# Kernel optimization log

Hardware: AMD Instinct MI355X
Metric: run time of the kernel (lower is better)

The kernel has to match this reference:

```python
import jax, jax.numpy as jnp
import numpy as np
import math

B, S, HID, H, WBAND = 2, 4096, 768, 12, 128
D = HID // H  # 64


def _band_qk(q, k, w):
    """q,k: [B,S,H,D] -> banded scores [B,S,H,2w+1] (offset d -> key pos i+d-w)."""
    b, s, h, d = q.shape
    nc = s // w
    kp = jnp.pad(k, ((0, 0), (w, w), (0, 0), (0, 0)))  # zero padding_value
    idx = (jnp.arange(nc) * w)[:, None] + jnp.arange(3 * w)[None, :]  # [nc,3w]
    kw = kp[:, idx]                                   # [B,nc,3w,H,D]
    qc = q.reshape(b, nc, w, h, d)
    scores = jnp.einsum('bcxhd,bcyhd->bchxy', qc, kw)  # [B,nc,H,w,3w]
    # extract diagonals: P[x,dd] = scores[x, x+dd] via flatten/skew trick
    flat = scores.reshape(b, nc, h, w * 3 * w)
    flat = jnp.pad(flat, ((0, 0), (0, 0), (0, 0), (0, w)))
    diag = flat.reshape(b, nc, h, w, 3 * w + 1)[..., : 2 * w + 1]
    return diag.transpose(0, 1, 3, 2, 4).reshape(b, s, h, 2 * w + 1)


def _band_pv(p, v, w):
    """p: [B,S,H,2w+1], v: [B,S,H,D] -> context [B,S,H,D]."""
    b, s, h, k = p.shape
    d = v.shape[-1]
    nc = s // w
    vp = jnp.pad(v, ((0, 0), (w, w), (0, 0), (0, 0)))
    idx = (jnp.arange(nc) * w)[:, None] + jnp.arange(3 * w)[None, :]
    vw = vp[:, idx]                                   # [B,nc,3w,H,D]
    pc = p.reshape(b, nc, w, h, k).transpose(0, 1, 3, 2, 4)  # [B,nc,H,w,2w+1]
    pc = jnp.pad(pc, ((0, 0), (0, 0), (0, 0), (0, 0), (0, w)))  # [..,w,3w+1]
    band = pc.reshape(b, nc, h, w * (3 * w + 1))[..., : w * 3 * w]
    band = band.reshape(b, nc, h, w, 3 * w)           # M[x, x+dd] = p[x,dd]
    ctx = jnp.einsum('bchxy,bcyhd->bcxhd', band, vw)  # [B,nc,w,H,D]
    return ctx.reshape(b, s, h, d)


def setup_inputs() -> dict:
    key = jax.random.key(0)
    ks = jax.random.split(key, 8)
    init = lambda k, shp: (jax.random.normal(k, shp, jnp.float32) * 0.02)
    return {
        'x': jax.random.normal(ks[0], (B, S, HID), jnp.float32),
        'Wq': init(ks[1], (HID, HID)), 'bq': jnp.zeros((HID,), jnp.float32),
        'Wk': init(ks[2], (HID, HID)), 'bk': jnp.zeros((HID,), jnp.float32),
        'Wv': init(ks[3], (HID, HID)), 'bv': jnp.zeros((HID,), jnp.float32),
        'Wd': init(ks[4], (H, D, HID)), 'bd': jnp.zeros((HID,), jnp.float32),
        'gamma': jnp.ones((HID,), jnp.float32),
        'beta': jnp.zeros((HID,), jnp.float32),
    }


def reference(x, Wq, bq, Wk, bk, Wv, bv, Wd, bd, gamma, beta):
    w = WBAND
    b, s, _ = x.shape
    q = (x @ Wq + bq).reshape(b, s, H, D) / math.sqrt(D)
    k = (x @ Wk + bk).reshape(b, s, H, D)
    v = (x @ Wv + bv).reshape(b, s, H, D)
    scores = _band_qk(q, k, w)                        # [B,S,H,2w+1]
    # mask_invalid_locations: key pos i + d - w must lie in [0, S)
    pos = jnp.arange(s)[:, None] + jnp.arange(2 * w + 1)[None, :] - w
    valid = (pos >= 0) & (pos < s)                    # [S,2w+1]
    scores = jnp.where(valid[None, :, None, :], scores, -1e9)
    probs = jax.nn.softmax(scores, axis=-1)           # float32 softmax
    ctx = _band_pv(probs, v, w)                       # [B,S,H,D]
    proj = jnp.einsum('bfnd,ndh->bfh', ctx, Wd) + bd  # output projection
    y = x + proj                                      # residual (dropout=0)
    mu = jnp.mean(y, axis=-1, keepdims=True)
    var = jnp.mean(jnp.square(y - mu), axis=-1, keepdims=True)
    out = (y - mu) / jnp.sqrt(var + 1e-12) * gamma + beta
    return out
```

## Files before the change

### kernel.cpp

```cpp
#include <hip/hip_runtime.h>
#include <math.h>

typedef unsigned short u16;
typedef __bf16 bf16x8 __attribute__((ext_vector_type(8)));
typedef float f32x4 __attribute__((ext_vector_type(4)));

constexpr int Bc   = 2;
constexpr int Sc   = 4096;
constexpr int HIDc = 768;
constexpr int Hc   = 12;
constexpr int Dc   = 64;
constexpr int Wc   = 128;
constexpr int Mc   = Bc * Sc;

constexpr int QT2  = 64;
constexpr int WIN  = QT2 + 2 * Wc;
constexpr int NCT  = WIN / 16;

static __device__ __forceinline__ void load_lds16(const void* g, void* l) {
    __builtin_amdgcn_global_load_lds(
        (const __attribute__((address_space(1))) void*)g,
        (__attribute__((address_space(3))) void*)l, 16, 0, 0);
}
static __device__ __forceinline__ u16 to_bf16(float f) {
    return __builtin_bit_cast(u16, (__bf16)f);
}

__global__ __launch_bounds__(256) void prep_x(const float* __restrict__ x,
                                              u16* __restrict__ xb,
                                              u16* __restrict__ zpad)
{
    int i = blockIdx.x * 256 + threadIdx.x;
    float4 v = ((const float4*)x)[i];
    ushort4 o;
    o.x = to_bf16(v.x); o.y = to_bf16(v.y);
    o.z = to_bf16(v.z); o.w = to_bf16(v.w);
    ((ushort4*)xb)[i] = o;
    if (blockIdx.x == 0 && threadIdx.x < 128)
        ((int4*)zpad)[threadIdx.x] = make_int4(0, 0, 0, 0);
}

__global__ __launch_bounds__(256) void prep_w(
    const float* __restrict__ Wq, const float* __restrict__ Wk,
    const float* __restrict__ Wv, const float* __restrict__ Wd,
    u16* __restrict__ wqt, u16* __restrict__ wkt,
    u16* __restrict__ wvt, u16* __restrict__ wdt)
{
    const int z = blockIdx.z;
    const float* W = z == 0 ? Wq : z == 1 ? Wk : z == 2 ? Wv : Wd;
    u16* T         = z == 0 ? wqt : z == 1 ? wkt : z == 2 ? wvt : wdt;

    __shared__ float t[32][33];
    const int bx = blockIdx.x * 32, by = blockIdx.y * 32;
    const int tx = threadIdx.x & 31, ty = threadIdx.x >> 5;
#pragma unroll
    for (int i = 0; i < 32; i += 8)
        t[ty + i][tx] = W[(size_t)(by + ty + i) * HIDc + bx + tx];
    __syncthreads();
#pragma unroll
    for (int i = 0; i < 32; i += 8)
        T[(size_t)(bx + ty + i) * HIDc + by + tx] = to_bf16(t[tx][ty + i]);
}

__device__ __forceinline__ void gemm128_bt(
    const u16* __restrict__ A, const u16* __restrict__ Bt,
    int m0, int n0, u16* As, u16* Bs, f32x4 (&acc)[4][4])
{
    const int tid  = threadIdx.x;
    const int lane = tid & 63, wid = tid >> 6;
    const int c16  = lane & 15, g = lane >> 4;
    const int wm   = (wid >> 1) * 64, wn = (wid & 1) * 64;
    const int soff = wid * 4096 + lane * 16;

    for (int k0 = 0; k0 < HIDc; k0 += 64) {
        __syncthreads();
#pragma unroll
        for (int i = 0; i < 4; ++i) {
            int off  = soff + i * 1024;
            int row  = off >> 7;
            int slot = (off >> 4) & 7;
            int seg  = slot ^ (row & 7);
            load_lds16(A  + (size_t)(m0 + row) * HIDc + k0 + seg * 8, (char*)As + off);
            load_lds16(Bt + (size_t)(n0 + row) * HIDc + k0 + seg * 8, (char*)Bs + off);
        }
        __syncthreads();
#pragma unroll
        for (int kk = 0; kk < 2; ++kk) {
            bf16x8 af[4], bfr[4];
#pragma unroll
            for (int t = 0; t < 4; ++t) {
                int ar = wm + t * 16 + c16;
                int as = (kk * 4 + g) ^ (ar & 7);
                af[t]  = *(const bf16x8*)(As + ar * 64 + as * 8);
                int br = wn + t * 16 + c16;
                int bs = (kk * 4 + g) ^ (br & 7);
                bfr[t] = *(const bf16x8*)(Bs + br * 64 + bs * 8);
            }
#pragma unroll
            for (int mt = 0; mt < 4; ++mt)
#pragma unroll
                for (int nt = 0; nt < 4; ++nt)
                    acc[mt][nt] = __builtin_amdgcn_mfma_f32_16x16x32_bf16(
                        af[mt], bfr[nt], acc[mt][nt], 0, 0, 0);
        }
    }
}

__global__ __launch_bounds__(256) void gemm_qkv_mfma(
    const u16* __restrict__ xb,
    const u16* __restrict__ wqt, const u16* __restrict__ wkt,
    const u16* __restrict__ wvt,
    const float* __restrict__ bq, const float* __restrict__ bk,
    const float* __restrict__ bv,
    u16* __restrict__ qg, u16* __restrict__ kg, u16* __restrict__ vtg)
{
    __shared__ u16 As[128 * 64], Bs[128 * 64];
    const int z = blockIdx.z;
    const u16* Bt     = z == 0 ? wqt : z == 1 ? wkt : wvt;
    const float* bias = z == 0 ? bq : z == 1 ? bk : bv;
    const float scale = z == 0 ? 0.125f : 1.0f;
    u16* outqk        = z == 0 ? qg : kg;

    const int m0 = blockIdx.x * 128, n0 = blockIdx.y * 128;
    f32x4 acc[4][4];
#pragma unroll
    for (int i = 0; i < 4; ++i)
#pragma unroll
        for (int j = 0; j < 4; ++j) acc[i][j] = (f32x4){0.f, 0.f, 0.f, 0.f};

    gemm128_bt(xb, Bt, m0, n0, As, Bs, acc);

    const int tid = threadIdx.x, lane = tid & 63, wid = tid >> 6;
    const int c16 = lane & 15, g = lane >> 4;
    const int wm = (wid >> 1) * 64, wn = (wid & 1) * 64;

#pragma unroll
    for (int nt = 0; nt < 4; ++nt) {
        int n = n0 + wn + nt * 16 + c16;
        int h = n >> 6, d = n & 63;
        float bn = bias[n];
#pragma unroll
        for (int mt = 0; mt < 4; ++mt) {
            int m = m0 + wm + mt * 16 + g * 4;
            int b = m >> 12, s = m & (Sc - 1);
            if (z == 2) {
                size_t base = ((size_t)(b * Hc + h)) * Sc * Dc + (size_t)d * Sc + s;
                ushort4 pk;
                pk.x = to_bf16(acc[mt][nt][0] + bn);
                pk.y = to_bf16(acc[mt][nt][1] + bn);
                pk.z = to_bf16(acc[mt][nt][2] + bn);
                pk.w = to_bf16(acc[mt][nt][3] + bn);
                *(ushort4*)&vtg[base] = pk;
            } else {
                size_t base = ((size_t)(b * Hc + h)) * Sc * Dc + (size_t)s * Dc + d;
#pragma unroll
                for (int r = 0; r < 4; ++r)
                    outqk[base + (size_t)r * Dc] =
                        to_bf16((acc[mt][nt][r] + bn) * scale);
            }
        }
    }
}

__global__ __launch_bounds__(256) void gemm_proj_mfma(
    const u16* __restrict__ ctxb, const u16* __restrict__ wdt,
    const float* __restrict__ bd, const float* __restrict__ x,
    float* __restrict__ y)
{
    __shared__ u16 As[128 * 64], Bs[128 * 64];
    const int m0 = blockIdx.x * 128, n0 = blockIdx.y * 128;
    f32x4 acc[4][4];
#pragma unroll
    for (int i = 0; i < 4; ++i)
#pragma unroll
        for (int j = 0; j < 4; ++j) acc[i][j] = (f32x4){0.f, 0.f, 0.f, 0.f};

    gemm128_bt(ctxb, wdt, m0, n0, As, Bs, acc);

    const int tid = threadIdx.x, lane = tid & 63, wid = tid >> 6;
    const int c16 = lane & 15, g = lane >> 4;
    const int wm = (wid >> 1) * 64, wn = (wid & 1) * 64;

#pragma unroll
    for (int nt = 0; nt < 4; ++nt) {
        int n = n0 + wn + nt * 16 + c16;
        float bn = bd[n];
#pragma unroll
        for (int mt = 0; mt < 4; ++mt) {
#pragma unroll
            for (int r = 0; r < 4; ++r) {
                int m = m0 + wm + mt * 16 + g * 4 + r;
                size_t idx = (size_t)m * HIDc + n;
                y[idx] = acc[mt][nt][r] + bn + x[idx];
            }
        }
    }
}

__global__ __launch_bounds__(256) void band_attn_mfma(
    const u16* __restrict__ qg, const u16* __restrict__ kg,
    const u16* __restrict__ vtg, const u16* __restrict__ zpad,
    u16* __restrict__ ctxb)
{
    extern __shared__ u16 sm[];
    u16* kwin = sm;
    u16* vt   = sm + 20480;
    u16* pm   = sm;

    const int qc = blockIdx.x, h = blockIdx.y, b = blockIdx.z;
    const int s0 = qc * QT2;
    const int tid = threadIdx.x;
    const int lane = tid & 63, wid = tid >> 6;
    const int c16 = lane & 15, g = lane >> 4;
    const size_t hb = ((size_t)(b * Hc + h)) * Sc * Dc;

#pragma unroll
    for (int i = 0; i < 10; ++i) {
        int c   = i * 4 + wid;
        int row = c * 8 + (lane >> 3);
        int seg = (lane & 7) ^ (lane >> 3);
        int pos = s0 - Wc + row;
        const u16* src = (pos >= 0 && pos < Sc)
                       ? &kg[hb + (size_t)pos * Dc + seg * 8] : zpad;
        load_lds16(src, (char*)kwin + c * 1024 + (lane & 63) * 16);
    }
#pragma unroll
    for (int i = 0; i < 10; ++i) {
        int c   = i * 4 + wid;
        int idx = c * 64 + lane;
        int d   = idx / 40;
        int p   = idx - d * 40;
        int seg = (p & 0x38) | ((p ^ d) & 7);
        int pos0 = s0 - Wc + seg * 8;
        const u16* src = (pos0 >= 0 && pos0 < Sc)
                       ? &vtg[hb + (size_t)d * Sc + pos0] : zpad;
        load_lds16(src, (char*)vt + idx * 16);
    }

    const u16* qp = &qg[hb + (size_t)(s0 + wid * 16 + c16) * Dc + g * 8];
    bf16x8 qa0 = *(const bf16x8*)qp;
    bf16x8 qa1 = *(const bf16x8*)(qp + 32);

    __syncthreads();

    f32x4 acc[NCT];
#pragma unroll
    for (int ct = 0; ct < NCT; ++ct) acc[ct] = (f32x4){0.f, 0.f, 0.f, 0.f};
    __builtin_amdgcn_s_setprio(1);
#pragma unroll
    for (int ct = 0; ct < NCT; ++ct) {
        int row = ct * 16 + c16;
        const u16* kb = kwin + row * 64;
        bf16x8 kb0 = *(const bf16x8*)(kb + (g       ^ (row & 7)) * 8);
        bf16x8 kb1 = *(const bf16x8*)(kb + ((g + 4) ^ (row & 7)) * 8);
        acc[ct] = __builtin_amdgcn_mfma_f32_16x16x32_bf16(qa0, kb0, acc[ct], 0, 0, 0);
        acc[ct] = __builtin_amdgcn_mfma_f32_16x16x32_bf16(qa1, kb1, acc[ct], 0, 0, 0);
    }
    __builtin_amdgcn_s_setprio(0);

    float mrow[4] = {-3e38f, -3e38f, -3e38f, -3e38f};
#pragma unroll
    for (int ct = 0; ct < NCT; ++ct) {
#pragma unroll
        for (int r = 0; r < 4; ++r) {
            int rl  = wid * 16 + g * 4 + r;
            int j   = ct * 16 + c16;
            int pos = s0 - Wc + j;
            bool valid = (j >= rl) && (j <= rl + 2 * Wc) && (pos >= 0) && (pos < Sc);
            float v = valid ? acc[ct][r] : -3e38f;
            acc[ct][r] = v;
            mrow[r] = fmaxf(mrow[r], v);
        }
    }
#pragma unroll
    for (int r = 0; r < 4; ++r)
#pragma unroll
        for (int off = 1; off < 16; off <<= 1)
            mrow[r] = fmaxf(mrow[r], __shfl_xor(mrow[r], off));

    float srow[4] = {0.f, 0.f, 0.f, 0.f};
#pragma unroll
    for (int ct = 0; ct < NCT; ++ct)
#pragma unroll
        for (int r = 0; r < 4; ++r) {
            float e = __expf(acc[ct][r] - mrow[r]);
            acc[ct][r] = e;
            srow[r] += e;
        }
#pragma unroll
    for (int r = 0; r < 4; ++r)
#pragma unroll
        for (int off = 1; off < 16; off <<= 1)
            srow[r] += __shfl_xor(srow[r], off);

    __syncthreads();

#pragma unroll
    for (int ct = 0; ct < NCT; ++ct)
#pragma unroll
        for (int r = 0; r < 4; ++r) {
            int q   = wid * 16 + g * 4 + r;
            int col = ct * 16 + c16;
            int sl  = col >> 3;
            int ph  = (sl & 0x38) | ((sl ^ q ^ (q >> 3)) & 7);
            pm[q * 320 + ph * 8 + (col & 7)] = to_bf16(acc[ct][r]);
        }

    f32x4 o[4];
#pragma unroll
    for (int dt = 0; dt < 4; ++dt) o[dt] = (f32x4){0.f, 0.f, 0.f, 0.f};
    const int qrow = wid * 16 + c16;
    __builtin_amdgcn_s_setprio(1);
#pragma unroll
    for (int ks = 0; ks < 10; ++ks) {
        int sl = ks * 4 + g;
        int ph = (sl & 0x38) | ((sl ^ qrow ^ (qrow >> 3)) & 7);
        bf16x8 pa = *(const bf16x8*)(pm + qrow * 320 + ph * 8);
#pragma unroll
        for (int dt = 0; dt < 4; ++dt) {
            int d  = dt * 16 + c16;
            int pv = (sl & 0x38) | ((sl ^ d) & 7);
            bf16x8 vb = *(const bf16x8*)(vt + d * 320 + pv * 8);
            o[dt] = __builtin_amdgcn_mfma_f32_16x16x32_bf16(pa, vb, o[dt], 0, 0, 0);
        }
    }
    __builtin_amdgcn_s_setprio(0);

    float inv[4];
#pragma unroll
    for (int r = 0; r < 4; ++r) inv[r] = 1.f / srow[r];
#pragma unroll
    for (int dt = 0; dt < 4; ++dt)
#pragma unroll
        for (int r = 0; r < 4; ++r) {
            int rl = wid * 16 + g * 4 + r;
            ctxb[((size_t)(b * Sc + s0 + rl)) * HIDc + h * Dc + dt * 16 + c16] =
                to_bf16(o[dt][r] * inv[r]);
        }
}

__global__ __launch_bounds__(256) void ln_kernel(
    const float* __restrict__ y,
    const float* __restrict__ gamma, const float* __restrict__ beta,
    float* __restrict__ out)
{
    const int m = blockIdx.x;
    const float* row = y + (size_t)m * HIDc;
    const int t = threadIdx.x;
    float v0 = row[t], v1 = row[t + 256], v2 = row[t + 512];
    float s = v0 + v1 + v2;
    __shared__ float red[4];
    const int lane = t & 63, wid = t >> 6;
#pragma unroll
    for (int o = 1; o < 64; o <<= 1) s += __shfl_xor(s, o);
    if (lane == 0) red[wid] = s;
    __syncthreads();
    const float mu = (red[0] + red[1] + red[2] + red[3]) * (1.f / HIDc);
    v0 -= mu; v1 -= mu; v2 -= mu;
    float s2 = v0 * v0 + v1 * v1 + v2 * v2;
#pragma unroll
    for (int o = 1; o < 64; o <<= 1) s2 += __shfl_xor(s2, o);
    __syncthreads();
    if (lane == 0) red[wid] = s2;
    __syncthreads();
    const float var = (red[0] + red[1] + red[2] + red[3]) * (1.f / HIDc);
    const float rstd = rsqrtf(var + 1e-12f);
    const size_t base = (size_t)m * HIDc;
    out[base + t]       = v0 * rstd * gamma[t]       + beta[t];
    out[base + t + 256] = v1 * rstd * gamma[t + 256] + beta[t + 256];
    out[base + t + 512] = v2 * rstd * gamma[t + 512] + beta[t + 512];
}

extern "C" void kernel_launch(void* const* d_in, const int* in_sizes, int n_in,
                              void* d_out, int out_size, void* d_ws, size_t ws_size,
                              hipStream_t stream)
{
    const float* x     = (const float*)d_in[0];
    const float* Wq    = (const float*)d_in[1];
    const float* bq    = (const float*)d_in[2];
    const float* Wk    = (const float*)d_in[3];
    const float* bk    = (const float*)d_in[4];
    const float* Wv    = (const float*)d_in[5];
    const float* bv    = (const float*)d_in[6];
    const float* Wd    = (const float*)d_in[7];
    const float* bd    = (const float*)d_in[8];
    const float* gamma = (const float*)d_in[9];
    const float* beta  = (const float*)d_in[10];
    float* out = (float*)d_out;

    constexpr size_t CHUNK = (size_t)Mc * HIDc;
    constexpr size_t WSZ   = (size_t)HIDc * HIDc;
    u16* xb   = (u16*)d_ws;
    u16* wqt  = xb + CHUNK;
    u16* wkt  = wqt + WSZ;
    u16* wvt  = wkt + WSZ;
    u16* wdt  = wvt + WSZ;
    u16* qg   = wdt + WSZ;
    u16* kg   = qg + CHUNK;
    u16* vtg  = kg + CHUNK;
    u16* ctxb = vtg + CHUNK;
    float* yws = (float*)(ctxb + CHUNK);
    u16* zpad  = (u16*)(yws + CHUNK);

    prep_x<<<(CHUNK / 4) / 256, 256, 0, stream>>>(x, xb, zpad);
    prep_w<<<dim3(24, 24, 4), 256, 0, stream>>>(Wq, Wk, Wv, Wd, wqt, wkt, wvt, wdt);

    gemm_qkv_mfma<<<dim3(Mc / 128, HIDc / 128, 3), 256, 0, stream>>>(
        xb, wqt, wkt, wvt, bq, bk, bv, qg, kg, vtg);

    band_attn_mfma<<<dim3(Sc / QT2, Hc, Bc), 256, 81920, stream>>>(
        qg, kg, vtg, zpad, ctxb);

    gemm_proj_mfma<<<dim3(Mc / 128, HIDc / 128), 256, 0, stream>>>(
        ctxb, wdt, bd, x, yws);

    ln_kernel<<<Mc, 256, 0, stream>>>(yws, gamma, beta, out);
}
```

Measured before the change: 134.0 us.

## Double-buffer GEMM K-loop, transpose MFMA outputs for vector stores, remap attention grid

The GEMM core now stages K-tiles of 32 into double-buffered LDS, prefetching the next tile while MFMAs run on the current one. This halves the barriers per K step and overlaps global loads with compute, and it raises wave priority around the MFMA block. The Q/K and projection GEMMs swap MFMA operands so each lane holds four consecutive columns, which lets the epilogues write vectorised ushort4/float4 stores and the V GEMM moves to its own kernel. The attention kernel uses a flattened grid that groups head/batch pairs per XCD for L2 locality, and it swaps PV operands so context rows are written as packed vectors. The cost is more index math and a softmax-sum shuffle.

```diff
diff --git a/kernel.cpp b/kernel.cpp
--- a/kernel.cpp
+++ b/kernel.cpp
@@ -62,64 +62,78 @@
         T[(size_t)(bx + ty + i) * HIDc + by + tx] = to_bf16(t[tx][ty + i]);
 }
 
-__device__ __forceinline__ void gemm128_bt(
+__device__ __forceinline__ void stage_tile(const u16* __restrict__ M,
+                                           int r0, int k0, u16* lds)
+{
+    const int tid = threadIdx.x;
+#pragma unroll
+    for (int i = 0; i < 2; ++i) {
+        int u    = tid + i * 256;
+        int pair = u >> 3, phys = u & 7;
+        int s8   = phys ^ (pair & 7);
+        int row  = 2 * pair + (s8 >> 2);
+        int kseg = s8 & 3;
+        load_lds16(M + (size_t)(r0 + row) * HIDc + k0 + kseg * 8,
+                   (char*)lds + u * 16);
+    }
+}
+
+template <int SWAP>
+__device__ __forceinline__ void gemm128_core(
     const u16* __restrict__ A, const u16* __restrict__ Bt,
     int m0, int n0, u16* As, u16* Bs, f32x4 (&acc)[4][4])
 {
-    const int tid  = threadIdx.x;
-    const int lane = tid & 63, wid = tid >> 6;
-    const int c16  = lane & 15, g = lane >> 4;
-    const int wm   = (wid >> 1) * 64, wn = (wid & 1) * 64;
-    const int soff = wid * 4096 + lane * 16;
-
-    for (int k0 = 0; k0 < HIDc; k0 += 64) {
+    const int lane = threadIdx.x & 63, wid = threadIdx.x >> 6;
+    const int c16 = lane & 15, g = lane >> 4;
+    const int wm = (wid >> 1) * 64, wn = (wid & 1) * 64;
+
+    stage_tile(A,  m0, 0, As);
+    stage_tile(Bt, n0, 0, Bs);
+    __syncthreads();
+    int cur = 0;
+    for (int t = 0; t < 24; ++t) {
+        if (t + 1 < 24) {
+            stage_tile(A,  m0, (t + 1) * 32, As + (cur ^ 1) * 4096);
+            stage_tile(Bt, n0, (t + 1) * 32, Bs + (cur ^ 1) * 4096);
+        }
+        bf16x8 af[4], bfr[4];
+#pragma unroll
+        for (int tt = 0; tt < 4; ++tt) {
+            int ar = wm + tt * 16 + c16;
+            int ap = ar >> 1, a8 = (((ar & 1) << 2) | g) ^ (ap & 7);
+            af[tt] = *(const bf16x8*)(As + cur * 4096 + ap * 64 + a8 * 8);
+            int br = wn + tt * 16 + c16;
+            int bp = br >> 1, b8 = (((br & 1) << 2) | g) ^ (bp & 7);
+            bfr[tt] = *(const bf16x8*)(Bs + cur * 4096 + bp * 64 + b8 * 8);
+        }
+        __builtin_amdgcn_s_setprio(1);
+#pragma unroll
+        for (int mt = 0; mt < 4; ++mt)
+#pragma unroll
+            for (int nt = 0; nt < 4; ++nt)
+                acc[mt][nt] = SWAP
+                    ? __builtin_amdgcn_mfma_f32_16x16x32_bf16(
+                          bfr[nt], af[mt], acc[mt][nt], 0, 0, 0)
+                    : __builtin_amdgcn_mfma_f32_16x16x32_bf16(
+                          af[mt], bfr[nt], acc[mt][nt], 0, 0, 0);
+        __builtin_amdgcn_s_setprio(0);
         __syncthreads();
-#pragma unroll
-        for (int i = 0; i < 4; ++i) {
-            int off  = soff + i * 1024;
-            int row  = off >> 7;
-            int slot = (off >> 4) & 7;
-            int seg  = slot ^ (row & 7);
-            load_lds16(A  + (size_t)(m0 + row) * HIDc + k0 + seg * 8, (char*)As + off);
-            load_lds16(Bt + (size_t)(n0 + row) * HIDc + k0 + seg * 8, (char*)Bs + off);
-        }
-        __syncthreads();
-#pragma unroll
-        for (int kk = 0; kk < 2; ++kk) {
-            bf16x8 af[4], bfr[4];
-#pragma unroll
-            for (int t = 0; t < 4; ++t) {
-                int ar = wm + t * 16 + c16;
-                int as = (kk * 4 + g) ^ (ar & 7);
-                af[t]  = *(const bf16x8*)(As + ar * 64 + as * 8);
-                int br = wn + t * 16 + c16;
-                int bs = (kk * 4 + g) ^ (br & 7);
-                bfr[t] = *(const bf16x8*)(Bs + br * 64 + bs * 8);
-            }
-#pragma unroll
-            for (int mt = 0; mt < 4; ++mt)
-#pragma unroll
-                for (int nt = 0; nt < 4; ++nt)
-                    acc[mt][nt] = __builtin_amdgcn_mfma_f32_16x16x32_bf16(
-                        af[mt], bfr[nt], acc[mt][nt], 0, 0, 0);
-        }
-    }
-}
-
-__global__ __launch_bounds__(256) void gemm_qkv_mfma(
+        cur ^= 1;
+    }
+}
+
+__global__ __launch_bounds__(256) void gemm_qk_mfma(
     const u16* __restrict__ xb,
     const u16* __restrict__ wqt, const u16* __restrict__ wkt,
-    const u16* __restrict__ wvt,
     const float* __restrict__ bq, const float* __restrict__ bk,
-    const float* __restrict__ bv,
-    u16* __restrict__ qg, u16* __restrict__ kg, u16* __restrict__ vtg)
-{
-    __shared__ u16 As[128 * 64], Bs[128 * 64];
+    u16* __restrict__ qg, u16* __restrict__ kg)
+{
+    __shared__ u16 As[8192], Bs[8192];
     const int z = blockIdx.z;
-    const u16* Bt     = z == 0 ? wqt : z == 1 ? wkt : wvt;
-    const float* bias = z == 0 ? bq : z == 1 ? bk : bv;
-    const float scale = z == 0 ? 0.125f : 1.0f;
-    u16* outqk        = z == 0 ? qg : kg;
+    const u16* Bt     = z ? wkt : wqt;
+    const float* bias = z ? bk : bq;
+    const float scale = z ? 1.0f : 0.125f;
+    u16* outp         = z ? kg : qg;
 
     const int m0 = blockIdx.x * 128, n0 = blockIdx.y * 128;
     f32x4 acc[4][4];
@@ -128,9 +142,47 @@
 #pragma unroll
         for (int j = 0; j < 4; ++j) acc[i][j] = (f32x4){0.f, 0.f, 0.f, 0.f};
 
-    gemm128_bt(xb, Bt, m0, n0, As, Bs, acc);
-
-    const int tid = threadIdx.x, lane = tid & 63, wid = tid >> 6;
+    gemm128_core<1>(xb, Bt, m0, n0, As, Bs, acc);
+
+    const int lane = threadIdx.x & 63, wid = threadIdx.x >> 6;
+    const int c16 = lane & 15, g = lane >> 4;
+    const int wm = (wid >> 1) * 64, wn = (wid & 1) * 64;
+
+#pragma unroll
+    for (int mt = 0; mt < 4; ++mt) {
+        int m = m0 + wm + mt * 16 + c16;
+        int b = m >> 12, s = m & (Sc - 1);
+        size_t rowbase = (size_t)(b * Hc) * Sc * Dc + (size_t)s * Dc;
+#pragma unroll
+        for (int nt = 0; nt < 4; ++nt) {
+            int nb = n0 + wn + nt * 16 + g * 4;
+            int h = nb >> 6, d0 = nb & 63;
+            float4 b4 = *(const float4*)&bias[nb];
+            ushort4 pk;
+            pk.x = to_bf16((acc[mt][nt][0] + b4.x) * scale);
+            pk.y = to_bf16((acc[mt][nt][1] + b4.y) * scale);
+            pk.z = to_bf16((acc[mt][nt][2] + b4.z) * scale);
+            pk.w = to_bf16((acc[mt][nt][3] + b4.w) * scale);
+            *(ushort4*)&outp[rowbase + (size_t)h * Sc * Dc + d0] = pk;
+        }
+    }
+}
+
+__global__ __launch_bounds__(256) void gemm_v_mfma(
+    const u16* __restrict__ xb, const u16* __restrict__ wvt,
+    const float* __restrict__ bv, u16* __restrict__ vtg)
+{
+    __shared__ u16 As[8192], Bs[8192];
+    const int m0 = blockIdx.x * 128, n0 = blockIdx.y * 128;
+    f32x4 acc[4][4];
+#pragma unroll
+    for (int i = 0; i < 4; ++i)
+#pragma unroll
+        for (int j = 0; j < 4; ++j) acc[i][j] = (f32x4){0.f, 0.f, 0.f, 0.f};
+
+    gemm128_core<0>(xb, wvt, m0, n0, As, Bs, acc);
+
+    const int lane = threadIdx.x & 63, wid = threadIdx.x >> 6;
     const int c16 = lane & 15, g = lane >> 4;
     const int wm = (wid >> 1) * 64, wn = (wid & 1) * 64;
 
@@ -138,26 +190,18 @@
     for (int nt = 0; nt < 4; ++nt) {
         int n = n0 + wn + nt * 16 + c16;
         int h = n >> 6, d = n & 63;
-        float bn = bias[n];
+        float bn = bv[n];
 #pragma unroll
         for (int mt = 0; mt < 4; ++mt) {
             int m = m0 + wm + mt * 16 + g * 4;
             int b = m >> 12, s = m & (Sc - 1);
-            if (z == 2) {
-                size_t base = ((size_t)(b * Hc + h)) * Sc * Dc + (size_t)d * Sc + s;
-                ushort4 pk;
-                pk.x = to_bf16(acc[mt][nt][0] + bn);
-                pk.y = to_bf16(acc[mt][nt][1] + bn);
-                pk.z = to_bf16(acc[mt][nt][2] + bn);
-                pk.w = to_bf16(acc[mt][nt][3] + bn);
-                *(ushort4*)&vtg[base] = pk;
-            } else {
-                size_t base = ((size_t)(b * Hc + h)) * Sc * Dc + (size_t)s * Dc + d;
-#pragma unroll
-                for (int r = 0; r < 4; ++r)
-                    outqk[base + (size_t)r * Dc] =
-                        to_bf16((acc[mt][nt][r] + bn) * scale);
-            }
+            size_t base = ((size_t)(b * Hc + h)) * Sc * Dc + (size_t)d * Sc + s;
+            ushort4 pk;
+            pk.x = to_bf16(acc[mt][nt][0] + bn);
+            pk.y = to_bf16(acc[mt][nt][1] + bn);
+            pk.z = to_bf16(acc[mt][nt][2] + bn);
+            pk.w = to_bf16(acc[mt][nt][3] + bn);
+            *(ushort4*)&vtg[base] = pk;
         }
     }
 }
@@ -167,7 +211,7 @@
     const float* __restrict__ bd, const float* __restrict__ x,
     float* __restrict__ y)
 {
-    __shared__ u16 As[128 * 64], Bs[128 * 64];
+    __shared__ u16 As[8192], Bs[8192];
     const int m0 = blockIdx.x * 128, n0 = blockIdx.y * 128;
     f32x4 acc[4][4];
 #pragma unroll
@@ -175,24 +219,26 @@
 #pragma unroll
         for (int j = 0; j < 4; ++j) acc[i][j] = (f32x4){0.f, 0.f, 0.f, 0.f};
 
-    gemm128_bt(ctxb, wdt, m0, n0, As, Bs, acc);
-
-    const int tid = threadIdx.x, lane = tid & 63, wid = tid >> 6;
+    gemm128_core<1>(ctxb, wdt, m0, n0, As, Bs, acc);
+
+    const int lane = threadIdx.x & 63, wid = threadIdx.x >> 6;
     const int c16 = lane & 15, g = lane >> 4;
     const int wm = (wid >> 1) * 64, wn = (wid & 1) * 64;
 
 #pragma unroll
-    for (int nt = 0; nt < 4; ++nt) {
-        int n = n0 + wn + nt * 16 + c16;
-        float bn = bd[n];
-#pragma unroll
-        for (int mt = 0; mt < 4; ++mt) {
-#pragma unroll
-            for (int r = 0; r < 4; ++r) {
-                int m = m0 + wm + mt * 16 + g * 4 + r;
-                size_t idx = (size_t)m * HIDc + n;
-                y[idx] = acc[mt][nt][r] + bn + x[idx];
-            }
+    for (int mt = 0; mt < 4; ++mt) {
+        int m = m0 + wm + mt * 16 + c16;
+#pragma unroll
+        for (int nt = 0; nt < 4; ++nt) {
+            int nb = n0 + wn + nt * 16 + g * 4;
+            float4 b4 = *(const float4*)&bd[nb];
+            float4 x4 = *(const float4*)&x[(size_t)m * HIDc + nb];
+            float4 o4;
+            o4.x = acc[mt][nt][0] + b4.x + x4.x;
+            o4.y = acc[mt][nt][1] + b4.y + x4.y;
+            o4.z = acc[mt][nt][2] + b4.z + x4.z;
+            o4.w = acc[mt][nt][3] + b4.w + x4.w;
+            *(float4*)&y[(size_t)m * HIDc + nb] = o4;
         }
     }
 }
@@ -207,12 +253,17 @@
     u16* vt   = sm + 20480;
     u16* pm   = sm;
 
-    const int qc = blockIdx.x, h = blockIdx.y, b = blockIdx.z;
+    const int L = blockIdx.x;
+    const int xcd = L & 7, tt = L >> 3;
+    const int hb = xcd * 3 + (tt % 3);
+    const int qc = tt / 3;
+    const int h = hb % Hc, b = hb / Hc;
+
     const int s0 = qc * QT2;
     const int tid = threadIdx.x;
     const int lane = tid & 63, wid = tid >> 6;
     const int c16 = lane & 15, g = lane >> 4;
-    const size_t hb = ((size_t)(b * Hc + h)) * Sc * Dc;
+    const size_t hbase = ((size_t)(b * Hc + h)) * Sc * Dc;
 
 #pragma unroll
     for (int i = 0; i < 10; ++i) {
@@ -221,7 +272,7 @@
         int seg = (lane & 7) ^ (lane >> 3);
         int pos = s0 - Wc + row;
         const u16* src = (pos >= 0 && pos < Sc)
-                       ? &kg[hb + (size_t)pos * Dc + seg * 8] : zpad;
+                       ? &kg[hbase + (size_t)pos * Dc + seg * 8] : zpad;
         load_lds16(src, (char*)kwin + c * 1024 + (lane & 63) * 16);
     }
 #pragma unroll
@@ -233,11 +284,11 @@
         int seg = (p & 0x38) | ((p ^ d) & 7);
         int pos0 = s0 - Wc + seg * 8;
         const u16* src = (pos0 >= 0 && pos0 < Sc)
-                       ? &vtg[hb + (size_t)d * Sc + pos0] : zpad;
+                       ? &vtg[hbase + (size_t)d * Sc + pos0] : zpad;
         load_lds16(src, (char*)vt + idx * 16);
     }
 
-    const u16* qp = &qg[hb + (size_t)(s0 + wid * 16 + c16) * Dc + g * 8];
+    const u16* qp = &qg[hbase + (size_t)(s0 + wid * 16 + c16) * Dc + g * 8];
     bf16x8 qa0 = *(const bf16x8*)qp;
     bf16x8 qa1 = *(const bf16x8*)(qp + 32);
 
@@ -306,6 +357,14 @@
             pm[q * 320 + ph * 8 + (col & 7)] = to_bf16(acc[ct][r]);
         }
 
+    float sq0 = __shfl(srow[0], (c16 >> 2) << 4);
+    float sq1 = __shfl(srow[1], (c16 >> 2) << 4);
+    float sq2 = __shfl(srow[2], (c16 >> 2) << 4);
+    float sq3 = __shfl(srow[3], (c16 >> 2) << 4);
+    int rr = c16 & 3;
+    float sq = rr == 0 ? sq0 : rr == 1 ? sq1 : rr == 2 ? sq2 : sq3;
+    float invq = 1.f / sq;
+
     f32x4 o[4];
 #pragma unroll
     for (int dt = 0; dt < 4; ++dt) o[dt] = (f32x4){0.f, 0.f, 0.f, 0.f};
@@ -321,22 +380,21 @@
             int d  = dt * 16 + c16;
             int pv = (sl & 0x38) | ((sl ^ d) & 7);
             bf16x8 vb = *(const bf16x8*)(vt + d * 320 + pv * 8);
-            o[dt] = __builtin_amdgcn_mfma_f32_16x16x32_bf16(pa, vb, o[dt], 0, 0, 0);
+            o[dt] = __builtin_amdgcn_mfma_f32_16x16x32_bf16(vb, pa, o[dt], 0, 0, 0);
         }
     }
     __builtin_amdgcn_s_setprio(0);
 
-    float inv[4];
-#pragma unroll
-    for (int r = 0; r < 4; ++r) inv[r] = 1.f / srow[r];
-#pragma unroll
-    for (int dt = 0; dt < 4; ++dt)
-#pragma unroll
-        for (int r = 0; r < 4; ++r) {
-            int rl = wid * 16 + g * 4 + r;
-            ctxb[((size_t)(b * Sc + s0 + rl)) * HIDc + h * Dc + dt * 16 + c16] =
-                to_bf16(o[dt][r] * inv[r]);
-        }
+    const size_t crow = ((size_t)(b * Sc + s0 + wid * 16 + c16)) * HIDc + h * Dc;
+#pragma unroll
+    for (int dt = 0; dt < 4; ++dt) {
+        ushort4 pk;
+        pk.x = to_bf16(o[dt][0] * invq);
+        pk.y = to_bf16(o[dt][1] * invq);
+        pk.z = to_bf16(o[dt][2] * invq);
+        pk.w = to_bf16(o[dt][3] * invq);
+        *(ushort4*)&ctxb[crow + dt * 16 + g * 4] = pk;
+    }
 }
 
 __global__ __launch_bounds__(256) void ln_kernel(
@@ -405,10 +463,12 @@
     prep_x<<<(CHUNK / 4) / 256, 256, 0, stream>>>(x, xb, zpad);
     prep_w<<<dim3(24, 24, 4), 256, 0, stream>>>(Wq, Wk, Wv, Wd, wqt, wkt, wvt, wdt);
 
-    gemm_qkv_mfma<<<dim3(Mc / 128, HIDc / 128, 3), 256, 0, stream>>>(
-        xb, wqt, wkt, wvt, bq, bk, bv, qg, kg, vtg);
-
-    band_attn_mfma<<<dim3(Sc / QT2, Hc, Bc), 256, 81920, stream>>>(
+    gemm_qk_mfma<<<dim3(Mc / 128, HIDc / 128, 2), 256, 0, stream>>>(
+        xb, wqt, wkt, bq, bk, qg, kg);
+    gemm_v_mfma<<<dim3(Mc / 128, HIDc / 128), 256, 0, stream>>>(
+        xb, wvt, bv, vtg);
+
+    band_attn_mfma<<<dim3(Sc / QT2 * Hc * Bc), 256, 81920, stream>>>(
         qg, kg, vtg, zpad, ctxb);
 
     gemm_proj_mfma<<<dim3(Mc / 128, HIDc / 128), 256, 0, stream>>>(
```

Measured after the change: 144.3 us. 7.7% more time.
